# Performance work log

Measured on AMD Instinct MI355X. Metric: run time of the kernel, lower is better.

The kernel has to match this reference:

```python
import jax, jax.numpy as jnp
import numpy as np

NEG_SLOPE = 0.2  # PyG GATConv default leaky_relu slope
BN_EPS = 1e-5


def gat_conv(x, src, dst, num_nodes, W, a_src, a_dst, bias, concat):
    """PyG-style GATConv (eval mode, self-loops already appended to src/dst)."""
    H, F = a_src.shape
    h = (x @ W).reshape(num_nodes, H, F)              # [N,H,F]
    e_src = jnp.einsum('nhf,hf->nh', h, a_src)        # [N,H]
    e_dst = jnp.einsum('nhf,hf->nh', h, a_dst)        # [N,H]
    e = jax.nn.leaky_relu(e_src[src] + e_dst[dst], NEG_SLOPE)  # [E,H]
    m = jax.ops.segment_max(e, dst, num_segments=num_nodes)    # segment softmax (stable)
    w = jnp.exp(e - m[dst])
    z = jax.ops.segment_sum(w, dst, num_segments=num_nodes)
    alpha = w / (z[dst] + 1e-16)                      # [E,H]
    msg = alpha[:, :, None] * h[src]                  # [E,H,F]
    out = jax.ops.segment_sum(msg, dst, num_segments=num_nodes)  # [N,H,F]
    out = out.reshape(num_nodes, H * F) if concat else out.mean(axis=1)
    return out + bias


def bn_eval(x, gamma, beta):
    # BatchNorm1d eval with initialized running stats (mean=0, var=1)
    return x * (gamma / jnp.sqrt(1.0 + BN_EPS)) + beta


def setup_inputs() -> dict:
    key = jax.random.key(0)
    ks = jax.random.split(key, 16)
    N, E, Fin, H, Fh, MLP = 50000, 800000, 128, 4, 32, 64
    HF = H * Fh  # 128
    s = 0.05
    inp = {
        'x': jax.random.normal(ks[0], (N, Fin), jnp.float32),
        'edge_index': jax.random.randint(ks[1], (2, E), 0, N, jnp.int64),
        # conv0: Fin -> Fh per head, concat
        'W1': jax.random.normal(ks[2], (Fin, HF), jnp.float32) * s,
        'a1s': jax.random.normal(ks[3], (H, Fh), jnp.float32) * s,
        'a1d': jax.random.normal(ks[4], (H, Fh), jnp.float32) * s,
        'b1': jnp.zeros((HF,), jnp.float32),
        # conv1: HF -> Fh per head, concat
        'W2': jax.random.normal(ks[5], (HF, HF), jnp.float32) * s,
        'a2s': jax.random.normal(ks[6], (H, Fh), jnp.float32) * s,
        'a2d': jax.random.normal(ks[7], (H, Fh), jnp.float32) * s,
        'b2': jnp.zeros((HF,), jnp.float32),
        # mlp block 0
        'M1w': jax.random.normal(ks[8], (HF, MLP), jnp.float32) * s,
        'M1b': jnp.zeros((MLP,), jnp.float32),
        'g1': jnp.ones((MLP,), jnp.float32),
        'be1': jnp.zeros((MLP,), jnp.float32),
        'M2w': jax.random.normal(ks[9], (MLP, HF), jnp.float32) * s,
        'M2b': jnp.zeros((HF,), jnp.float32),
        'g2': jnp.ones((HF,), jnp.float32),
        'be2': jnp.zeros((HF,), jnp.float32),
        # conv2: HF -> Fh per head, mean over heads (concat=False)
        'W3': jax.random.normal(ks[10], (HF, HF), jnp.float32) * s,
        'a3s': jax.random.normal(ks[11], (H, Fh), jnp.float32) * s,
        'a3d': jax.random.normal(ks[12], (H, Fh), jnp.float32) * s,
        'b3': jnp.zeros((Fh,), jnp.float32),
    }
    return inp


def reference(x, edge_index, W1, a1s, a1d, b1, W2, a2s, a2d, b2,
              M1w, M1b, g1, be1, M2w, M2b, g2, be2, W3, a3s, a3d, b3):
    N = x.shape[0]
    loops = jnp.arange(N, dtype=edge_index.dtype)
    src = jnp.concatenate([edge_index[0], loops])  # add self-loops (PyG default)
    dst = jnp.concatenate([edge_index[1], loops])

    # layer 0: conv -> relu -> (dropout=id, eval) -> mlp[0]
    h = jax.nn.relu(gat_conv(x, src, dst, N, W1, a1s, a1d, b1, concat=True))
    h = bn_eval(jax.nn.relu(h @ M1w + M1b), g1, be1)
    h = bn_eval(jax.nn.relu(h @ M2w + M2b), g2, be2)

    # layer 1: conv -> relu -> (dropout=id)
    h = jax.nn.relu(gat_conv(h, src, dst, N, W2, a2s, a2d, b2, concat=True))

    # output layer: concat=False -> mean over heads
    out = gat_conv(h, src, dst, N, W3, a3s, a3d, b3, concat=False)
    return out
```

## Files before the change

kernel.cpp:

```cpp
#include <hip/hip_runtime.h>
#include <hip/hip_bf16.h>

#define NEG_SLOPE 0.2f
#define BN_RS 0.9999950000374997f

typedef __attribute__((ext_vector_type(8))) _Float16 f16x8;
typedef __attribute__((ext_vector_type(2))) _Float16 f16x2;
typedef __attribute__((ext_vector_type(4))) float f32x4;

__device__ __forceinline__ void store_split(float w, _Float16* H, _Float16* L, size_t off) {
  _Float16 h = (_Float16)w;
  H[off] = h;
  L[off] = (_Float16)(w - (float)h);
}


__global__ void eb_hist(const int* __restrict__ ei, int* __restrict__ bucketSize, int E) {
  __shared__ int h[256];
  int tid = threadIdx.x;
  h[tid] = 0;
  __syncthreads();
  for (int i = blockIdx.x * 256 + tid; i < E; i += gridDim.x * 256)
    atomicAdd(&h[ei[E + i] >> 8], 1);
  __syncthreads();
  if (h[tid]) atomicAdd(&bucketSize[tid], h[tid]);
}

__global__ void eb_scan(const int* __restrict__ bucketSize, int* __restrict__ edgeStart,
                        int* __restrict__ cursor, int* __restrict__ csrStart, int N) {
  __shared__ int sd[256];
  int tid = threadIdx.x;
  int v = bucketSize[tid];
  sd[tid] = v;
  __syncthreads();
  for (int off = 1; off < 256; off <<= 1) {
    int t = (tid >= off) ? sd[tid - off] : 0;
    __syncthreads();
    sd[tid] += t;
    __syncthreads();
  }
  int excl = sd[tid] - v;
  edgeStart[tid] = excl;
  cursor[tid] = excl;
  csrStart[tid] = excl + min(tid << 8, N);
  if (tid == 255) edgeStart[256] = sd[255];
}

#define PCH 4096
__global__ __launch_bounds__(256) void eb_part(const int* __restrict__ ei,
                                               int* __restrict__ cursor,
                                               unsigned* __restrict__ staging, int E) {
  __shared__ unsigned val[PCH];
  __shared__ unsigned char bk[PCH];
  __shared__ int cnt[256];
  __shared__ int base[256];
  int tid = threadIdx.x;
  cnt[tid] = 0;
  __syncthreads();
  int e0 = blockIdx.x * PCH;
  int n = min(PCH, E - e0);
  for (int j = tid; j < n; j += 256) {
    int s = ei[e0 + j], d = ei[E + e0 + j];
    val[j] = ((unsigned)(d & 255) << 16) | (unsigned)s;
    int b = d >> 8;
    bk[j] = (unsigned char)b;
    atomicAdd(&cnt[b], 1);
  }
  __syncthreads();
  if (cnt[tid]) base[tid] = atomicAdd(&cursor[tid], cnt[tid]);
  __syncthreads();
  for (int j = tid; j < n; j += 256) {
    int b = bk[j];
    int off = atomicSub(&cnt[b], 1) - 1;
    staging[base[b] + off] = val[j];
  }
}

__global__ __launch_bounds__(256) void eb_csr(
    const unsigned* __restrict__ staging, const int* __restrict__ edgeStart,
    const int* __restrict__ csrStart, int* __restrict__ rowptr,
    unsigned* __restrict__ csr, int N) {
  __shared__ int deg[256];
  __shared__ int sc[256];
  __shared__ int ex[256];
  int b = blockIdx.x, tid = threadIdx.x;
  int n0 = b << 8;
  int nn = min(256, N - n0);
  deg[tid] = (tid < nn) ? 1 : 0;
  __syncthreads();
  int s0 = edgeStart[b], s1 = edgeStart[b + 1];
  for (int j = s0 + tid; j < s1; j += 256)
    atomicAdd(&deg[staging[j] >> 16], 1);
  __syncthreads();
  int dv = deg[tid];
  sc[tid] = dv;
  __syncthreads();
  for (int off = 1; off < 256; off <<= 1) {
    int t = (tid >= off) ? sc[tid - off] : 0;
    __syncthreads();
    sc[tid] += t;
    __syncthreads();
  }
  int incl = sc[tid];
  int cbase = csrStart[b];
  ex[tid] = incl - dv;
  if (tid < nn) {
    rowptr[n0 + tid + 1] = cbase + incl;
    unsigned me = (unsigned)(n0 + tid);
    csr[cbase + incl - 1] = (me << 16) | me;
  }
  if (b == 0 && tid == 0) rowptr[0] = 0;
  deg[tid] = 0;
  __syncthreads();
  for (int j = s0 + tid; j < s1; j += 256) {
    unsigned v = staging[j];
    int dl = v >> 16;
    unsigned src = v & 0xFFFF;
    int off = atomicAdd(&deg[dl], 1);
    csr[cbase + ex[dl] + off] = ((unsigned)(n0 + dl) << 16) | src;
  }
}

__device__ __forceinline__ void wprep_conv(const float* __restrict__ W,
                                           const float* __restrict__ as_,
                                           const float* __restrict__ ad_,
                                           _Float16* __restrict__ H, _Float16* __restrict__ L,
                                           int lb, int tid) {
  if (lb < 64) {
    int idx = lb * 256 + tid;
    int k = idx >> 7, p = idx & 127;
    store_split(W[k * 128 + p], H, L, (size_t)p * 128 + k);
  } else if (lb < 68) {
    int idx = (lb - 64) * 256 + tid;
    int rl = idx >> 7, k = idx & 127;
    const float* a = (rl < 4) ? as_ : ad_;
    int h = rl & 3;
    float s = 0.f;
#pragma unroll
    for (int f = 0; f < 32; f++) s += W[k * 128 + h * 32 + f] * a[h * 32 + f];
    store_split(s, H, L, (size_t)(128 + rl) * 128 + k);
  } else {
    int idx = (lb - 68) * 256 + tid;
    int rl = idx >> 7, k = idx & 127;
    H[(size_t)(136 + rl) * 128 + k] = (_Float16)0.f;
    L[(size_t)(136 + rl) * 128 + k] = (_Float16)0.f;
  }
}

__global__ void wprep_all(
    const float* __restrict__ W1, const float* __restrict__ a1s, const float* __restrict__ a1d,
    _Float16* __restrict__ W1H, _Float16* __restrict__ W1L,
    const float* __restrict__ W2, const float* __restrict__ a2s, const float* __restrict__ a2d,
    _Float16* __restrict__ W2H, _Float16* __restrict__ W2L,
    const float* __restrict__ W3, const float* __restrict__ a3s, const float* __restrict__ a3d,
    _Float16* __restrict__ W3H, _Float16* __restrict__ W3L,
    const float* __restrict__ M1, _Float16* __restrict__ M1H, _Float16* __restrict__ M1L,
    const float* __restrict__ M2, _Float16* __restrict__ M2H, _Float16* __restrict__ M2L,
    int* __restrict__ bucketSize) {
  int b = blockIdx.x, tid = threadIdx.x;
  if (b < 72)       wprep_conv(W1, a1s, a1d, W1H, W1L, b, tid);
  else if (b < 144) wprep_conv(W2, a2s, a2d, W2H, W2L, b - 72, tid);
  else if (b < 216) wprep_conv(W3, a3s, a3d, W3H, W3L, b - 144, tid);
  else if (b < 248) {
    int idx = (b - 216) * 256 + tid;
    int k = idx >> 6, p = idx & 63;
    store_split(M1[k * 64 + p], M1H, M1L, (size_t)p * 128 + k);
  } else if (b < 280) {
    int idx = (b - 248) * 256 + tid;
    int k = idx >> 7, p = idx & 127;
    store_split(M2[k * 128 + p], M2H, M2L, (size_t)p * 64 + k);
  } else {
    bucketSize[tid] = 0;
  }
}

template <typename TA>
__global__ __launch_bounds__(256) void gemm_f16(
    const TA* __restrict__ A, const _Float16* __restrict__ WtH,
    const _Float16* __restrict__ WtL, _Float16* __restrict__ C, int N,
    float* __restrict__ esb, float* __restrict__ edb) {
  constexpr int PT = 144, PST = 128, K = 128;
  constexpr int CTB = 2;
  constexpr int KT = K / 32;
  __shared__ _Float16 As[128 * 32];
  __shared__ _Float16 WsH[PT * 32];
  __shared__ _Float16 WsL[PT * 32];
  const int tid = threadIdx.x;
  const int wave = tid >> 6, lane = tid & 63;
  const int quad = lane >> 4, l16 = lane & 15;
  const int row0 = blockIdx.x * 128;
  const bool xw = (wave == 0);

  f32x4 acc[8][CTB + 1];
#pragma unroll
  for (int rt = 0; rt < 8; rt++)
#pragma unroll
    for (int nt = 0; nt < CTB + 1; nt++) acc[rt][nt] = (f32x4){0.f, 0.f, 0.f, 0.f};

  for (int kc = 0; kc < KT; ++kc) {
    {
      int r = tid >> 1, part = tid & 1;
      int gr = row0 + r;
      _Float16* dst = &As[r * 32 + part * 16];
      if (gr < N) {
        const TA* src = A + (size_t)gr * K + kc * 32 + part * 16;
        if constexpr (sizeof(TA) == 4) {
          f16x8 h0, h1;
#pragma unroll
          for (int j = 0; j < 8; j++) { h0[j] = (_Float16)src[j]; h1[j] = (_Float16)src[8 + j]; }
          *(f16x8*)dst = h0; *(f16x8*)(dst + 8) = h1;
        } else {
          uint4 v0 = *(const uint4*)src;
          uint4 v1 = *(const uint4*)(src + 8);
          *(uint4*)dst = v0; *(uint4*)(dst + 8) = v1;
        }
      } else {
        *(uint4*)dst = make_uint4(0, 0, 0, 0);
        *(uint4*)(dst + 8) = make_uint4(0, 0, 0, 0);
      }
    }
    for (int idx = tid; idx < PT * 2; idx += 256) {
      int isL = idx >= PT;
      int p = isL ? idx - PT : idx;
      const _Float16* src = (isL ? WtL : WtH) + (size_t)p * K + kc * 32;
      _Float16* dst = (isL ? WsL : WsH) + p * 32;
      uint4 a0 = *(const uint4*)src;       uint4 a1 = *(const uint4*)(src + 8);
      uint4 a2 = *(const uint4*)(src + 16); uint4 a3 = *(const uint4*)(src + 24);
      *(uint4*)dst = a0; *(uint4*)(dst + 8) = a1;
      *(uint4*)(dst + 16) = a2; *(uint4*)(dst + 24) = a3;
    }
    __syncthreads();

    f16x8 bh[CTB], bl[CTB], bhE, blE;
#pragma unroll
    for (int nt = 0; nt < CTB; nt++) {
      int p = (wave * CTB + nt) * 16 + l16;
      bh[nt] = *(f16x8*)&WsH[p * 32 + quad * 8];
      bl[nt] = *(f16x8*)&WsL[p * 32 + quad * 8];
    }
    if (xw) {
      int p = 4 * CTB * 16 + l16;
      bhE = *(f16x8*)&WsH[p * 32 + quad * 8];
      blE = *(f16x8*)&WsL[p * 32 + quad * 8];
    }
#pragma unroll
    for (int rt = 0; rt < 8; rt++) {
      f16x8 a = *(f16x8*)&As[(rt * 16 + l16) * 32 + quad * 8];
#pragma unroll
      for (int nt = 0; nt < CTB; nt++) {
        acc[rt][nt] = __builtin_amdgcn_mfma_f32_16x16x32_f16(a, bh[nt], acc[rt][nt], 0, 0, 0);
        acc[rt][nt] = __builtin_amdgcn_mfma_f32_16x16x32_f16(a, bl[nt], acc[rt][nt], 0, 0, 0);
      }
      if (xw) {
        acc[rt][CTB] = __builtin_amdgcn_mfma_f32_16x16x32_f16(a, bhE, acc[rt][CTB], 0, 0, 0);
        acc[rt][CTB] = __builtin_amdgcn_mfma_f32_16x16x32_f16(a, blE, acc[rt][CTB], 0, 0, 0);
      }
    }
    __syncthreads();
  }

#pragma unroll
  for (int nt = 0; nt < CTB; nt++) {
    int c = (wave * CTB + nt) * 16 + l16;
#pragma unroll
    for (int rt = 0; rt < 8; rt++)
#pragma unroll
      for (int g = 0; g < 4; g++) {
        int r = row0 + rt * 16 + quad * 4 + g;
        if (r < N) C[(size_t)r * PST + c] = (_Float16)acc[rt][nt][g];
      }
  }
  if (wave == 0 && l16 < 8) {
    float* dstb = (l16 < 4) ? esb : edb;
    int h = l16 & 3;
#pragma unroll
    for (int rt = 0; rt < 8; rt++)
#pragma unroll
      for (int g = 0; g < 4; g++) {
        int r = row0 + rt * 16 + quad * 4 + g;
        if (r < N) dstb[(size_t)r * 4 + h] = acc[rt][CTB][g];
      }
  }
}

__global__ __launch_bounds__(256) void mlp_fused(
    const _Float16* __restrict__ A,
    const _Float16* __restrict__ M1H, const _Float16* __restrict__ M1L,
    const _Float16* __restrict__ M2H, const _Float16* __restrict__ M2L,
    _Float16* __restrict__ C, int N,
    const float* __restrict__ b1v, const float* __restrict__ g1v, const float* __restrict__ be1v,
    const float* __restrict__ b2v, const float* __restrict__ g2v, const float* __restrict__ be2v) {
  __shared__ _Float16 As[128 * 32];
  __shared__ _Float16 W1Hs[64 * 32], W1Ls[64 * 32];
  __shared__ _Float16 T[128 * 72];
  __shared__ _Float16 W2Hs[128 * 32], W2Ls[128 * 32];
  const int tid = threadIdx.x;
  const int wave = tid >> 6, lane = tid & 63;
  const int quad = lane >> 4, l16 = lane & 15;
  const int row0 = blockIdx.x * 128;

  f32x4 acc1[8];
#pragma unroll
  for (int rt = 0; rt < 8; rt++) acc1[rt] = (f32x4){0.f, 0.f, 0.f, 0.f};
  for (int kc = 0; kc < 4; ++kc) {
    {
      int r = tid >> 1, part = tid & 1;
      int gr = row0 + r;
      _Float16* dst = &As[r * 32 + part * 16];
      if (gr < N) {
        const _Float16* src = A + (size_t)gr * 128 + kc * 32 + part * 16;
        uint4 v0 = *(const uint4*)src;
        uint4 v1 = *(const uint4*)(src + 8);
        *(uint4*)dst = v0; *(uint4*)(dst + 8) = v1;
      } else {
        *(uint4*)dst = make_uint4(0, 0, 0, 0);
        *(uint4*)(dst + 8) = make_uint4(0, 0, 0, 0);
      }
    }
    if (tid < 128) {
      int isL = tid >= 64;
      int p = tid & 63;
      const _Float16* src = (isL ? M1L : M1H) + (size_t)p * 128 + kc * 32;
      _Float16* dst = (isL ? W1Ls : W1Hs) + p * 32;
      uint4 a0 = *(const uint4*)src;       uint4 a1 = *(const uint4*)(src + 8);
      uint4 a2 = *(const uint4*)(src + 16); uint4 a3 = *(const uint4*)(src + 24);
      *(uint4*)dst = a0; *(uint4*)(dst + 8) = a1;
      *(uint4*)(dst + 16) = a2; *(uint4*)(dst + 24) = a3;
    }
    __syncthreads();
    int p = wave * 16 + l16;
    f16x8 bh = *(f16x8*)&W1Hs[p * 32 + quad * 8];
    f16x8 bl = *(f16x8*)&W1Ls[p * 32 + quad * 8];
#pragma unroll
    for (int rt = 0; rt < 8; rt++) {
      f16x8 a = *(f16x8*)&As[(rt * 16 + l16) * 32 + quad * 8];
      acc1[rt] = __builtin_amdgcn_mfma_f32_16x16x32_f16(a, bh, acc1[rt], 0, 0, 0);
      acc1[rt] = __builtin_amdgcn_mfma_f32_16x16x32_f16(a, bl, acc1[rt], 0, 0, 0);
    }
    __syncthreads();
  }
  {
    int c = wave * 16 + l16;
    float bi = b1v[c], ga = g1v[c] * BN_RS, be = be1v[c];
#pragma unroll
    for (int rt = 0; rt < 8; rt++)
#pragma unroll
      for (int g = 0; g < 4; g++) {
        int r = rt * 16 + quad * 4 + g;
        float v = acc1[rt][g] + bi;
        v = v > 0.f ? v : 0.f;
        v = v * ga + be;
        T[r * 72 + c] = (_Float16)v;
      }
  }
  __syncthreads();

  f32x4 acc2[8][2];
#pragma unroll
  for (int rt = 0; rt < 8; rt++)
#pragma unroll
    for (int nt = 0; nt < 2; nt++) acc2[rt][nt] = (f32x4){0.f, 0.f, 0.f, 0.f};
  for (int kc = 0; kc < 2; ++kc) {
    {
      int isL = tid >= 128;
      int p = tid & 127;
      const _Float16* src = (isL ? M2L : M2H) + (size_t)p * 64 + kc * 32;
      _Float16* dst = (isL ? W2Ls : W2Hs) + p * 32;
      uint4 a0 = *(const uint4*)src;       uint4 a1 = *(const uint4*)(src + 8);
      uint4 a2 = *(const uint4*)(src + 16); uint4 a3 = *(const uint4*)(src + 24);
      *(uint4*)dst = a0; *(uint4*)(dst + 8) = a1;
      *(uint4*)(dst + 16) = a2; *(uint4*)(dst + 24) = a3;
    }
    __syncthreads();
    f16x8 bh[2], bl[2];
#pragma unroll
    for (int nt = 0; nt < 2; nt++) {
      int p = (wave * 2 + nt) * 16 + l16;
      bh[nt] = *(f16x8*)&W2Hs[p * 32 + quad * 8];
      bl[nt] = *(f16x8*)&W2Ls[p * 32 + quad * 8];
    }
#pragma unroll
    for (int rt = 0; rt < 8; rt++) {
      f16x8 a = *(f16x8*)&T[(rt * 16 + l16) * 72 + kc * 32 + quad * 8];
#pragma unroll
      for (int nt = 0; nt < 2; nt++) {
        acc2[rt][nt] = __builtin_amdgcn_mfma_f32_16x16x32_f16(a, bh[nt], acc2[rt][nt], 0, 0, 0);
        acc2[rt][nt] = __builtin_amdgcn_mfma_f32_16x16x32_f16(a, bl[nt], acc2[rt][nt], 0, 0, 0);
      }
    }
    __syncthreads();
  }
#pragma unroll
  for (int nt = 0; nt < 2; nt++) {
    int c = (wave * 2 + nt) * 16 + l16;
    float bi = b2v[c], ga = g2v[c] * BN_RS, be = be2v[c];
#pragma unroll
    for (int rt = 0; rt < 8; rt++)
#pragma unroll
      for (int g = 0; g < 4; g++) {
        int r = row0 + rt * 16 + quad * 4 + g;
        if (r < N) {
          float v = acc2[rt][nt][g] + bi;
          v = v > 0.f ? v : 0.f;
          v = v * ga + be;
          C[(size_t)r * 128 + c] = (_Float16)v;
        }
      }
  }
}

template <int MODE>
__global__ __launch_bounds__(256) void gat_agg(
    const _Float16* __restrict__ hx, const int* __restrict__ rowptr,
    const unsigned* __restrict__ csr, const float* __restrict__ es,
    const float* __restrict__ ed, const float* __restrict__ bias,
    void* __restrict__ outp, int N) {
  __shared__ float4 wbuf[4][4][2][17];
  __shared__ int    sbuf[4][4][2][16];
  const int tid = threadIdx.x;
  const int wave = tid >> 6, lane = tid & 63;
  const int g = lane >> 4, il = lane & 15;
  const int hd = il >> 2;
  const int nid = (blockIdx.x * 4 + wave) * 4 + g;
  const bool valid = (nid < N);
  int beg = 0, end = 0;
  if (valid) { beg = rowptr[nid]; end = rowptr[nid + 1]; }
  float4 edv = make_float4(0.f, 0.f, 0.f, 0.f);
  if (valid) edv = *(const float4*)(ed + (size_t)nid * 4);
  float acc[8];
#pragma unroll
  for (int r = 0; r < 8; r++) acc[r] = 0.f;
  float z = 0.f;
  const _Float16* hb = hx + il * 8;
  const int nch = (end - beg + 15) >> 4;

  {
    int m = end - beg; if (m > 16) m = 16;
    if (il < m) {
      int s = (int)(csr[beg + il] & 0xFFFFu);
      float4 e4 = *(const float4*)(es + (size_t)s * 4);
      float t0 = e4.x + edv.x, t1 = e4.y + edv.y;
      float t2 = e4.z + edv.z, t3 = e4.w + edv.w;
      t0 = t0 > 0.f ? t0 : NEG_SLOPE * t0;
      t1 = t1 > 0.f ? t1 : NEG_SLOPE * t1;
      t2 = t2 > 0.f ? t2 : NEG_SLOPE * t2;
      t3 = t3 > 0.f ? t3 : NEG_SLOPE * t3;
      wbuf[wave][g][0][il] = make_float4(__expf(t0), __expf(t1), __expf(t2), __expf(t3));
      sbuf[wave][g][0][il] = s;
    }
  }
  int pb = 0;
  for (int ci = 0; ci < nch; ++ci) {
    int c = beg + (ci << 4);
    int m = end - c; if (m > 16) m = 16;
    if (ci + 1 < nch) {
      int c2 = c + 16;
      int m2 = end - c2; if (m2 > 16) m2 = 16;
      if (il < m2) {
        int s = (int)(csr[c2 + il] & 0xFFFFu);
        float4 e4 = *(const float4*)(es + (size_t)s * 4);
        float t0 = e4.x + edv.x, t1 = e4.y + edv.y;
        float t2 = e4.z + edv.z, t3 = e4.w + edv.w;
        t0 = t0 > 0.f ? t0 : NEG_SLOPE * t0;
        t1 = t1 > 0.f ? t1 : NEG_SLOPE * t1;
        t2 = t2 > 0.f ? t2 : NEG_SLOPE * t2;
        t3 = t3 > 0.f ? t3 : NEG_SLOPE * t3;
        wbuf[wave][g][pb ^ 1][il] = make_float4(__expf(t0), __expf(t1), __expf(t2), __expf(t3));
        sbuf[wave][g][pb ^ 1][il] = s;
      }
    }
    const float* wp = (const float*)&wbuf[wave][g][pb][0];
    const int*   sp = &sbuf[wave][g][pb][0];
    int j = 0;
    for (; j + 4 <= m; j += 4) {
      int s0 = sp[j], s1 = sp[j + 1], s2 = sp[j + 2], s3 = sp[j + 3];
      float w0 = wp[(j + 0) * 4 + hd], w1 = wp[(j + 1) * 4 + hd];
      float w2 = wp[(j + 2) * 4 + hd], w3 = wp[(j + 3) * 4 + hd];
      f16x8 r0 = *(const f16x8*)(hb + (size_t)s0 * 128);
      f16x8 r1 = *(const f16x8*)(hb + (size_t)s1 * 128);
      f16x8 r2 = *(const f16x8*)(hb + (size_t)s2 * 128);
      f16x8 r3 = *(const f16x8*)(hb + (size_t)s3 * 128);
      z += (w0 + w1) + (w2 + w3);
#pragma unroll
      for (int r = 0; r < 8; r++) {
        float a = acc[r];
        a = fmaf(w0, (float)r0[r], a);
        a = fmaf(w1, (float)r1[r], a);
        a = fmaf(w2, (float)r2[r], a);
        a = fmaf(w3, (float)r3[r], a);
        acc[r] = a;
      }
    }
    for (; j < m; ++j) {
      int s = sp[j];
      float w = wp[j * 4 + hd];
      f16x8 rv = *(const f16x8*)(hb + (size_t)s * 128);
      z += w;
#pragma unroll
      for (int r = 0; r < 8; r++) acc[r] = fmaf(w, (float)rv[r], acc[r]);
    }
    pb ^= 1;
  }
  float inv = 1.f / (z + 1e-16f);
  if (MODE == 0) {
    f16x8 o;
#pragma unroll
    for (int r = 0; r < 8; r++) {
      float v = acc[r] * inv + bias[il * 8 + r];
      v = v > 0.f ? v : 0.f;
      o[r] = (_Float16)v;
    }
    if (valid) *(f16x8*)((_Float16*)outp + (size_t)nid * 128 + il * 8) = o;
  } else {
    float v[8];
#pragma unroll
    for (int r = 0; r < 8; r++) {
      float t = acc[r] * inv;
      t += __shfl_xor(t, 4);
      t += __shfl_xor(t, 8);
      v[r] = t;
    }
    if (valid && il < 4) {
      float4 o0, o1;
      o0.x = v[0] * 0.25f + bias[il * 8 + 0];
      o0.y = v[1] * 0.25f + bias[il * 8 + 1];
      o0.z = v[2] * 0.25f + bias[il * 8 + 2];
      o0.w = v[3] * 0.25f + bias[il * 8 + 3];
      o1.x = v[4] * 0.25f + bias[il * 8 + 4];
      o1.y = v[5] * 0.25f + bias[il * 8 + 5];
      o1.z = v[6] * 0.25f + bias[il * 8 + 6];
      o1.w = v[7] * 0.25f + bias[il * 8 + 7];
      *(float4*)((float*)outp + (size_t)nid * 32 + il * 8) = o0;
      *(float4*)((float*)outp + (size_t)nid * 32 + il * 8 + 4) = o1;
    }
  }
}

extern "C" void kernel_launch(void* const* d_in, const int* in_sizes, int n_in,
                              void* d_out, int out_size, void* d_ws, size_t ws_size,
                              hipStream_t stream) {
  const float* x   = (const float*)d_in[0];
  const int*   ei  = (const int*)d_in[1];
  const float* W1  = (const float*)d_in[2];
  const float* a1s = (const float*)d_in[3];
  const float* a1d = (const float*)d_in[4];
  const float* b1  = (const float*)d_in[5];
  const float* W2  = (const float*)d_in[6];
  const float* a2s = (const float*)d_in[7];
  const float* a2d = (const float*)d_in[8];
  const float* b2  = (const float*)d_in[9];
  const float* M1w = (const float*)d_in[10];
  const float* M1b = (const float*)d_in[11];
  const float* g1  = (const float*)d_in[12];
  const float* be1 = (const float*)d_in[13];
  const float* M2w = (const float*)d_in[14];
  const float* M2b = (const float*)d_in[15];
  const float* g2  = (const float*)d_in[16];
  const float* be2 = (const float*)d_in[17];
  const float* W3  = (const float*)d_in[18];
  const float* a3s = (const float*)d_in[19];
  const float* a3d = (const float*)d_in[20];
  const float* b3  = (const float*)d_in[21];

  const int N = in_sizes[0] / 128;
  const int E = in_sizes[1] / 2;
  const int S = E + N;

  char* w = (char*)d_ws;
  _Float16* bufA = (_Float16*)w; w += (size_t)N * 128 * 2;
  _Float16* bufB = (_Float16*)w; w += (size_t)N * 128 * 2;
  float* esb  = (float*)w; w += (size_t)N * 4 * 4;
  float* edb  = (float*)w; w += (size_t)N * 4 * 4;
  int* rowptr = (int*)w;   w += (size_t)(N + 1) * 4;
  unsigned* csr = (unsigned*)w; w += (size_t)S * 4;
  unsigned* staging = (unsigned*)w; w += (size_t)E * 4;
  int* bucketSize = (int*)w; w += 256 * 4;
  int* edgeStart  = (int*)w; w += 257 * 4;
  int* cursor     = (int*)w; w += 256 * 4;
  int* csrStart   = (int*)w; w += 256 * 4;
  _Float16* W1H = (_Float16*)w; w += 144 * 128 * 2;
  _Float16* W1L = (_Float16*)w; w += 144 * 128 * 2;
  _Float16* W2H = (_Float16*)w; w += 144 * 128 * 2;
  _Float16* W2L = (_Float16*)w; w += 144 * 128 * 2;
  _Float16* W3H = (_Float16*)w; w += 144 * 128 * 2;
  _Float16* W3L = (_Float16*)w; w += 144 * 128 * 2;
  _Float16* M1H = (_Float16*)w; w += 64 * 128 * 2;
  _Float16* M1L = (_Float16*)w; w += 64 * 128 * 2;
  _Float16* M2H = (_Float16*)w; w += 128 * 64 * 2;
  _Float16* M2L = (_Float16*)w; w += 128 * 64 * 2;

  const int gb = (N + 127) / 128;
  const int aggb = (N + 15) / 16;
  const int nbk = (N + 255) / 256;
  const int pbk = (E + PCH - 1) / PCH;

  wprep_all<<<281, 256, 0, stream>>>(W1, a1s, a1d, W1H, W1L,
                                     W2, a2s, a2d, W2H, W2L,
                                     W3, a3s, a3d, W3H, W3L,
                                     M1w, M1H, M1L, M2w, M2H, M2L, bucketSize);

  eb_hist<<<256, 256, 0, stream>>>(ei, bucketSize, E);
  eb_scan<<<1, 256, 0, stream>>>(bucketSize, edgeStart, cursor, csrStart, N);
  eb_part<<<pbk, 256, 0, stream>>>(ei, cursor, staging, E);
  eb_csr<<<nbk, 256, 0, stream>>>(staging, edgeStart, csrStart, rowptr, csr, N);

  gemm_f16<float><<<gb, 256, 0, stream>>>(x, W1H, W1L, bufA, N, esb, edb);
  gat_agg<0><<<aggb, 256, 0, stream>>>(bufA, rowptr, csr, esb, edb, b1, bufB, N);
  mlp_fused<<<gb, 256, 0, stream>>>(bufB, M1H, M1L, M2H, M2L, bufA, N,
                                    M1b, g1, be1, M2b, g2, be2);

  gemm_f16<_Float16><<<gb, 256, 0, stream>>>(bufA, W2H, W2L, bufB, N, esb, edb);
  gat_agg<0><<<aggb, 256, 0, stream>>>(bufB, rowptr, csr, esb, edb, b2, bufA, N);

  gemm_f16<_Float16><<<gb, 256, 0, stream>>>(bufA, W3H, W3L, bufB, N, esb, edb);
  gat_agg<1><<<aggb, 256, 0, stream>>>(bufB, rowptr, csr, esb, edb, b3, d_out, N);
}
```

Baseline: 322.6 us.

## Sort nodes by in-degree and aggregate in degree-descending order

Builds a degree histogram during CSR construction, scans it and scatters node ids into a permutation sorted by in-degree, highest first. The GAT aggregation kernels then map each 16-lane group to perm[idx] instead of the consecutive node id. The aim is to balance work across lanes in a wave and schedule heavy nodes first. The cost is two extra launches, global atomics, and scattered rowptr/ed/output accesses that lose sequential locality.

```diff
diff --git a/kernel.cpp b/kernel.cpp
--- a/kernel.cpp
+++ b/kernel.cpp
@@ -79,7 +79,7 @@
 __global__ __launch_bounds__(256) void eb_csr(
     const unsigned* __restrict__ staging, const int* __restrict__ edgeStart,
     const int* __restrict__ csrStart, int* __restrict__ rowptr,
-    unsigned* __restrict__ csr, int N) {
+    unsigned* __restrict__ csr, int* __restrict__ degHist, int N) {
   __shared__ int deg[256];
   __shared__ int sc[256];
   __shared__ int ex[256];
@@ -108,6 +108,7 @@
     rowptr[n0 + tid + 1] = cbase + incl;
     unsigned me = (unsigned)(n0 + tid);
     csr[cbase + incl - 1] = (me << 16) | me;
+    atomicAdd(&degHist[min(dv, 511)], 1);
   }
   if (b == 0 && tid == 0) rowptr[0] = 0;
   deg[tid] = 0;
@@ -118,6 +119,34 @@
     unsigned src = v & 0xFFFF;
     int off = atomicAdd(&deg[dl], 1);
     csr[cbase + ex[dl] + off] = ((unsigned)(n0 + dl) << 16) | src;
+  }
+}
+
+__global__ void nd_scan(const int* __restrict__ degHist, int* __restrict__ binPos) {
+  __shared__ int part[256];
+  int tid = threadIdx.x;
+  int a = degHist[2 * tid], b = degHist[2 * tid + 1];
+  part[tid] = a + b;
+  __syncthreads();
+  for (int off = 1; off < 256; off <<= 1) {
+    int t = (tid >= off) ? part[tid - off] : 0;
+    __syncthreads();
+    part[tid] += t;
+    __syncthreads();
+  }
+  int excl = part[tid] - (a + b);
+  binPos[2 * tid] = excl;
+  binPos[2 * tid + 1] = excl + a;
+}
+
+__global__ void nd_scatter(const int* __restrict__ rowptr, int* binPos,
+                           int* __restrict__ perm, int N) {
+  int i = blockIdx.x * 256 + threadIdx.x;
+  if (i < N) {
+    int d = rowptr[i + 1] - rowptr[i];
+    if (d > 511) d = 511;
+    int pos = atomicAdd(&binPos[d], 1);
+    perm[N - 1 - pos] = i;
   }
 }
 
@@ -156,7 +185,7 @@
     _Float16* __restrict__ W3H, _Float16* __restrict__ W3L,
     const float* __restrict__ M1, _Float16* __restrict__ M1H, _Float16* __restrict__ M1L,
     const float* __restrict__ M2, _Float16* __restrict__ M2H, _Float16* __restrict__ M2L,
-    int* __restrict__ bucketSize) {
+    int* __restrict__ bucketSize, int* __restrict__ degHist) {
   int b = blockIdx.x, tid = threadIdx.x;
   if (b < 72)       wprep_conv(W1, a1s, a1d, W1H, W1L, b, tid);
   else if (b < 144) wprep_conv(W2, a2s, a2d, W2H, W2L, b - 72, tid);
@@ -171,6 +200,8 @@
     store_split(M2[k * 128 + p], M2H, M2L, (size_t)p * 64 + k);
   } else {
     bucketSize[tid] = 0;
+    degHist[tid] = 0;
+    degHist[256 + tid] = 0;
   }
 }
 
@@ -412,17 +443,18 @@
 template <int MODE>
 __global__ __launch_bounds__(256) void gat_agg(
     const _Float16* __restrict__ hx, const int* __restrict__ rowptr,
-    const unsigned* __restrict__ csr, const float* __restrict__ es,
-    const float* __restrict__ ed, const float* __restrict__ bias,
-    void* __restrict__ outp, int N) {
+    const unsigned* __restrict__ csr, const int* __restrict__ perm,
+    const float* __restrict__ es, const float* __restrict__ ed,
+    const float* __restrict__ bias, void* __restrict__ outp, int N) {
   __shared__ float4 wbuf[4][4][2][17];
   __shared__ int    sbuf[4][4][2][16];
   const int tid = threadIdx.x;
   const int wave = tid >> 6, lane = tid & 63;
   const int g = lane >> 4, il = lane & 15;
   const int hd = il >> 2;
-  const int nid = (blockIdx.x * 4 + wave) * 4 + g;
-  const bool valid = (nid < N);
+  const int idx = (blockIdx.x * 4 + wave) * 4 + g;
+  const bool valid = (idx < N);
+  const int nid = valid ? perm[idx] : 0;
   int beg = 0, end = 0;
   if (valid) { beg = rowptr[nid]; end = rowptr[nid + 1]; }
   float4 edv = make_float4(0.f, 0.f, 0.f, 0.f);
@@ -574,10 +606,13 @@
   int* rowptr = (int*)w;   w += (size_t)(N + 1) * 4;
   unsigned* csr = (unsigned*)w; w += (size_t)S * 4;
   unsigned* staging = (unsigned*)w; w += (size_t)E * 4;
+  int* perm   = (int*)w;   w += (size_t)N * 4;
   int* bucketSize = (int*)w; w += 256 * 4;
   int* edgeStart  = (int*)w; w += 257 * 4;
   int* cursor     = (int*)w; w += 256 * 4;
   int* csrStart   = (int*)w; w += 256 * 4;
+  int* degHist    = (int*)w; w += 512 * 4;
+  int* binPos     = (int*)w; w += 512 * 4;
   _Float16* W1H = (_Float16*)w; w += 144 * 128 * 2;
   _Float16* W1L = (_Float16*)w; w += 144 * 128 * 2;
   _Float16* W2H = (_Float16*)w; w += 144 * 128 * 2;
@@ -597,21 +632,25 @@
   wprep_all<<<281, 256, 0, stream>>>(W1, a1s, a1d, W1H, W1L,
                                      W2, a2s, a2d, W2H, W2L,
                                      W3, a3s, a3d, W3H, W3L,
-                                     M1w, M1H, M1L, M2w, M2H, M2L, bucketSize);
+                                     M1w, M1H, M1L, M2w, M2H, M2L,
+                                     bucketSize, degHist);
 
   eb_hist<<<256, 256, 0, stream>>>(ei, bucketSize, E);
   eb_scan<<<1, 256, 0, stream>>>(bucketSize, edgeStart, cursor, csrStart, N);
   eb_part<<<pbk, 256, 0, stream>>>(ei, cursor, staging, E);
-  eb_csr<<<nbk, 256, 0, stream>>>(staging, edgeStart, csrStart, rowptr, csr, N);
+  eb_csr<<<nbk, 256, 0, stream>>>(staging, edgeStart, csrStart, rowptr, csr, degHist, N);
+
+  nd_scan<<<1, 256, 0, stream>>>(degHist, binPos);
+  nd_scatter<<<nbk, 256, 0, stream>>>(rowptr, binPos, perm, N);
 
   gemm_f16<float><<<gb, 256, 0, stream>>>(x, W1H, W1L, bufA, N, esb, edb);
-  gat_agg<0><<<aggb, 256, 0, stream>>>(bufA, rowptr, csr, esb, edb, b1, bufB, N);
+  gat_agg<0><<<aggb, 256, 0, stream>>>(bufA, rowptr, csr, perm, esb, edb, b1, bufB, N);
   mlp_fused<<<gb, 256, 0, stream>>>(bufB, M1H, M1L, M2H, M2L, bufA, N,
                                     M1b, g1, be1, M2b, g2, be2);
 
   gemm_f16<_Float16><<<gb, 256, 0, stream>>>(bufA, W2H, W2L, bufB, N, esb, edb);
-  gat_agg<0><<<aggb, 256, 0, stream>>>(bufB, rowptr, csr, esb, edb, b2, bufA, N);
+  gat_agg<0><<<aggb, 256, 0, stream>>>(bufB, rowptr, csr, perm, esb, edb, b2, bufA, N);
 
   gemm_f16<_Float16><<<gb, 256, 0, stream>>>(bufA, W3H, W3L, bufB, N, esb, edb);
-  gat_agg<1><<<aggb, 256, 0, stream>>>(bufB, rowptr, csr, esb, edb, b3, d_out, N);
-}
+  gat_agg<1><<<aggb, 256, 0, stream>>>(bufB, rowptr, csr, perm, esb, edb, b3, d_out, N);
+}
```

Measured after the change: 596.8 us. 85.0% more time.
